# Kernel optimization log

Measured on AMD Instinct MI355X. Metric: run time of the kernel, lower is better.

Reference implementation:

```python
import jax, jax.numpy as jnp
import numpy as np

IN_F, OUT_F = 4096, 4096
IGS, OGS = 8, 1          # in_group_size, out_group_size
NCB, CBS = 1, 65536      # num_codebooks, codebook_size (2**16)
NIG, NOG = IN_F // IGS, OUT_F // OGS


def setup_inputs() -> dict:
    key = jax.random.key(0)
    k1, k2, k3, k4, k5 = jax.random.split(key, 5)
    x = jax.random.normal(k1, (4, 2048, IN_F), jnp.float32)
    codes = jax.random.randint(k2, (NOG, NIG, NCB), 0, CBS, dtype=jnp.int32)
    codebooks = jax.random.normal(k3, (NCB, CBS, OGS, IGS), jnp.float32) * 0.05
    scales = jax.random.uniform(k4, (NOG, 1, 1, 1), jnp.float32, 0.5, 1.5)
    bias = jax.random.normal(k5, (OUT_F,), jnp.float32) * 0.01
    return {"x": x, "codes": codes, "codebooks": codebooks, "scales": scales, "bias": bias}


def _dequantize_weight(codes, codebooks, scales):
    # codes: [nog, nig, ncb] int; codebooks: [ncb, cbs, ogs, igs]
    ncb, cbs, ogs, igs = codebooks.shape
    nog, nig, _ = codes.shape
    flat = codebooks.reshape(ncb, cbs, ogs * igs)
    # embedding_bag(mode='sum'): gather each codebook's vector and sum over codebooks
    gathered = flat[jnp.arange(ncb)[None, None, :], codes]  # [nog, nig, ncb, ogs*igs]
    w = gathered.sum(axis=2).reshape(nog, nig, ogs, igs)
    w = w * scales  # scales broadcasts over [nog, nig, ogs, igs]
    # [nog, nig, ogs, igs] -> [nog, ogs, nig, igs] -> [out_features, in_features]
    return w.swapaxes(1, 2).reshape(nog * ogs, nig * igs)


def reference(x, codes, codebooks, scales, bias):
    W = _dequantize_weight(codes, codebooks, scales)  # [OUT_F, IN_F]
    return x @ W.T + bias
```

## Files before the change

kernel.cpp:

```cpp
#include <hip/hip_runtime.h>
#include <hip/hip_bf16.h>

#define M_DIM 8192
#define N_DIM 4096
#define K_DIM 4096
#define NOG 4096
#define NIG 512

typedef __bf16 bf16x8 __attribute__((ext_vector_type(8)));
typedef float f32x16 __attribute__((ext_vector_type(16)));
typedef short short8 __attribute__((ext_vector_type(8)));

typedef const __attribute__((address_space(1))) void* as1_cvoid_p;
typedef __attribute__((address_space(3))) void* as3_void_p;

__device__ __forceinline__ unsigned short f2bf(float f) {
  union { float f; unsigned u; } c; c.f = f;
  unsigned u = c.u;
  return (unsigned short)((u + 0x7fffu + ((u >> 16) & 1u)) >> 16);
}

__global__ __launch_bounds__(256) void cvt_x_kernel(const float* __restrict__ x,
                                                    unsigned short* __restrict__ xb,
                                                    int n8) {
  int i = blockIdx.x * blockDim.x + threadIdx.x;
  int stride = gridDim.x * blockDim.x;
  for (; i < n8; i += stride) {
    const float4* p = (const float4*)(x) + (size_t)i * 2;
    float4 a = p[0], b = p[1];
    short8 o;
    o[0] = (short)f2bf(a.x); o[1] = (short)f2bf(a.y);
    o[2] = (short)f2bf(a.z); o[3] = (short)f2bf(a.w);
    o[4] = (short)f2bf(b.x); o[5] = (short)f2bf(b.y);
    o[6] = (short)f2bf(b.z); o[7] = (short)f2bf(b.w);
    ((short8*)xb)[i] = o;
  }
}

__global__ __launch_bounds__(256) void dequant_kernel(const int* __restrict__ codes,
                                                      const float* __restrict__ cb,
                                                      unsigned short* __restrict__ wb) {
  int idx = blockIdx.x * blockDim.x + threadIdx.x;
  int code = codes[idx];
  const float4* p = (const float4*)(cb + (size_t)code * 8);
  float4 a = p[0], b = p[1];
  short8 o;
  o[0] = (short)f2bf(a.x); o[1] = (short)f2bf(a.y);
  o[2] = (short)f2bf(a.z); o[3] = (short)f2bf(a.w);
  o[4] = (short)f2bf(b.x); o[5] = (short)f2bf(b.y);
  o[6] = (short)f2bf(b.z); o[7] = (short)f2bf(b.w);
  ((short8*)wb)[idx] = o;
}


#define BAR() __builtin_amdgcn_s_barrier()
#define SB() __builtin_amdgcn_sched_barrier(0)
#define PRIO1() __builtin_amdgcn_s_setprio(1)
#define PRIO0() __builtin_amdgcn_s_setprio(0)
#define LGKM(N_) asm volatile("s_waitcnt lgkmcnt(" #N_ ")" ::: "memory")
#define VMC(N_) asm volatile("s_waitcnt vmcnt(" #N_ ")" ::: "memory")

#define STAGE_P(G_, isB_, slot_, p_, kt_) do { \
  _Pragma("unroll") for (int i_ = 0; i_ < 2; ++i_) { \
    const unsigned short* src_ = (G_) + (size_t)sp_roff[i_] * 4096 + (unsigned)((kt_) + (p_) * 32) + spk; \
    __builtin_amdgcn_global_load_lds((as1_cvoid_p)src_, \
      (as3_void_p)(smem + (isB_) * 65536 + (slot_) * 32768 + (p_) * 16384 + spd[i_]), 16, 0, 0); \
  } } while (0)

#define LDA32(dst_, ks_, slot_) \
  _Pragma("unroll") for (int mf_ = 0; mf_ < 4; ++mf_) \
    dst_[mf_] = *(const bf16x8*)(smem + ((unsigned)((slot_) * 32768 + ((ks_) >> 1) * 16384 + mf_ * 2048 + aRd0) ^ (((ks_) & 1) << 5)));

#define LDB32(dst_, ks_, slot_) \
  _Pragma("unroll") for (int nf_ = 0; nf_ < 2; ++nf_) \
    dst_[nf_] = *(const bf16x8*)(smem + ((unsigned)(65536 + (slot_) * 32768 + ((ks_) >> 1) * 16384 + nf_ * 2048 + bRd0) ^ (((ks_) & 1) << 5)));

#define MFMA8(af_, bf_) \
  _Pragma("unroll") for (int mf_ = 0; mf_ < 4; ++mf_) \
  _Pragma("unroll") for (int nf_ = 0; nf_ < 2; ++nf_) \
    acc[mf_][nf_] = __builtin_amdgcn_mfma_f32_32x32x16_bf16(af_[mf_], bf_[nf_], acc[mf_][nf_], 0, 0, 0);

#define GROUP32(S_, MODE_, KT_) do { \
   \
  if ((MODE_) == 2) STAGE_P(Ag, 0, (S_) ^ 1, 0, (KT_) + 64); \
  LDA32(afA, 0, S_); LDB32(bfA, 0, S_); SB(); \
  LDA32(afB, 1, S_); LDB32(bfB, 1, S_); SB(); \
  LGKM(6); SB(); PRIO1(); MFMA8(afA, bfA); PRIO0(); SB(); \
   \
  if ((MODE_) == 2) STAGE_P(Bg, 1, (S_) ^ 1, 0, (KT_) + 64); \
  LGKM(0); SB(); PRIO1(); MFMA8(afB, bfB); PRIO0(); SB(); \
  if ((MODE_) == 2) { VMC(4); } else { VMC(0); } \
  BAR(); \
   \
  if ((MODE_) == 2) STAGE_P(Ag, 0, (S_) ^ 1, 1, (KT_) + 64); \
  LDA32(afA, 2, S_); LDB32(bfA, 2, S_); SB(); \
  LDA32(afB, 3, S_); LDB32(bfB, 3, S_); SB(); \
  LGKM(6); SB(); PRIO1(); MFMA8(afA, bfA); PRIO0(); SB(); \
   \
  if ((MODE_) == 2) STAGE_P(Bg, 1, (S_) ^ 1, 1, (KT_) + 64); \
  LGKM(0); SB(); PRIO1(); MFMA8(afB, bfB); PRIO0(); SB(); \
  if ((MODE_) == 2) { VMC(4); BAR(); } \
} while (0)

__global__ __launch_bounds__(512) void gemm8_kernel(
    const unsigned short* __restrict__ A,
    const unsigned short* __restrict__ B,
    const float* __restrict__ scales,
    const float* __restrict__ bias,
    float* __restrict__ C) {
  extern __shared__ char smem[];

  const int bid = blockIdx.x;
  const int swz = (bid & 7) * 64 + (bid >> 3);
  const int bm = swz >> 4;
  const int bn = swz & 15;

  const int tid = threadIdx.x;
  const int w = tid >> 6;
  const int l = tid & 63;
  const int wr = w >> 2;
  const int wcol = w & 3;

  const int llog3 = (l & 3) ^ (((l >> 5) & 1) << 1);
  const int spk = llog3 * 8;
  int sp_roff[2], spd[2];
#pragma unroll
  for (int i = 0; i < 2; ++i) {
    sp_roff[i] = w * 32 + i * 16 + (l >> 2);
    spd[i] = (w * 128 + i * 64 + l) * 16;
  }

  const unsigned short* Ag = A + (size_t)bm * 256 * 4096;
  const unsigned short* Bg = B + (size_t)bn * 256 * 4096;

  const int xr0 = ((l >> 5) * 16) + (((l >> 3) & 1) << 5);
  const int aRd0 = (wr * 128 + (l & 31)) * 64 + xr0;
  const int bRd0 = (wcol * 64 + (l & 31)) * 64 + xr0;

  f32x16 acc[4][2];
#pragma unroll
  for (int mf = 0; mf < 4; ++mf)
#pragma unroll
    for (int nf = 0; nf < 2; ++nf)
#pragma unroll
      for (int r = 0; r < 16; ++r) acc[mf][nf][r] = 0.f;

  bf16x8 afA[4], afB[4], bfA[2], bfB[2];

  STAGE_P(Ag, 0, 0, 0, 0); STAGE_P(Bg, 1, 0, 0, 0);
  STAGE_P(Ag, 0, 0, 1, 0); STAGE_P(Bg, 1, 0, 1, 0);
  VMC(4);
  BAR();

  int kt = 0;
  for (int j = 0; j < 31; ++j) {
    GROUP32(0, 2, kt);
    GROUP32(1, 2, kt + 64);
    kt += 128;
  }
  GROUP32(0, 2, 3968);
  GROUP32(1, 0, 4032);

  const int r0 = bm * 256 + wr * 128 + 4 * (l >> 5);
  const int c0 = bn * 256 + wcol * 64 + (l & 31);
#pragma unroll
  for (int nf = 0; nf < 2; ++nf) {
    const int col = c0 + nf * 32;
    const float s = scales[col];
    const float bv = bias[col];
#pragma unroll
    for (int mf = 0; mf < 4; ++mf) {
      f32x16 v = acc[mf][nf];
      const int rb = r0 + mf * 32;
#pragma unroll
      for (int r = 0; r < 16; ++r)
        C[(size_t)(rb + (r & 3) + 8 * (r >> 2)) * 4096 + col] = v[r] * s + bv;
    }
  }
}

extern "C" void kernel_launch(void* const* d_in, const int* in_sizes, int n_in,
                              void* d_out, int out_size, void* d_ws, size_t ws_size,
                              hipStream_t stream) {
  const float* x = (const float*)d_in[0];
  const int* codes = (const int*)d_in[1];
  const float* cb = (const float*)d_in[2];
  const float* scales = (const float*)d_in[3];
  const float* bias = (const float*)d_in[4];
  float* out = (float*)d_out;

  unsigned short* xb = (unsigned short*)d_ws;
  unsigned short* wb = (unsigned short*)((char*)d_ws + (size_t)M_DIM * K_DIM * 2);

  hipFuncSetAttribute((const void*)gemm8_kernel,
                      hipFuncAttributeMaxDynamicSharedMemorySize, 131072);

  cvt_x_kernel<<<4096, 256, 0, stream>>>(x, xb, (M_DIM * K_DIM) / 8);
  dequant_kernel<<<(NOG * NIG) / 256, 256, 0, stream>>>(codes, cb, wb);
  gemm8_kernel<<<dim3((M_DIM / 256) * (N_DIM / 256)), 512, 131072, stream>>>(
      xb, wb, scales, bias, out);
}
```

Measured before the change: 298.7 us.

## Restructure LDS layout into per-k-step slabs and software-pipeline fragment loads

Changes the shared-memory staging layout so each 16-wide k slice is stored as a contiguous slab, with rows indexed directly and no XOR swizzle. Global-to-LDS copies are split into four quarter stages interleaved with the four MFMA sub-steps. The first fragments of the next slot are prefetched before the last MFMA batch, so LDS reads overlap compute. This adds more barriers per group, and removing the swizzle may cause LDS bank conflicts on the read side.

```diff
diff --git a/kernel.cpp b/kernel.cpp
--- a/kernel.cpp
+++ b/kernel.cpp
@@ -60,20 +60,19 @@
 #define LGKM(N_) asm volatile("s_waitcnt lgkmcnt(" #N_ ")" ::: "memory")
 #define VMC(N_) asm volatile("s_waitcnt vmcnt(" #N_ ")" ::: "memory")
 
-#define STAGE_P(G_, isB_, slot_, p_, kt_) do { \
-  _Pragma("unroll") for (int i_ = 0; i_ < 2; ++i_) { \
-    const unsigned short* src_ = (G_) + (size_t)sp_roff[i_] * 4096 + (unsigned)((kt_) + (p_) * 32) + spk; \
-    __builtin_amdgcn_global_load_lds((as1_cvoid_p)src_, \
-      (as3_void_p)(smem + (isB_) * 65536 + (slot_) * 32768 + (p_) * 16384 + spd[i_]), 16, 0, 0); \
-  } } while (0)
+#define STAGE_I(G_, isB_, slot_, i_, kt_) do { \
+  const unsigned short* src_ = (G_) + (size_t)(srow0 + l) * 4096 + (unsigned)((kt_) + (i_) * 16 + shalf8); \
+  __builtin_amdgcn_global_load_lds((as1_cvoid_p)src_, \
+    (as3_void_p)(smem + (isB_) * 65536 + (slot_) * 32768 + ((i_) * 8 + w) * 1024), 16, 0, 0); \
+} while (0)
 
 #define LDA32(dst_, ks_, slot_) \
   _Pragma("unroll") for (int mf_ = 0; mf_ < 4; ++mf_) \
-    dst_[mf_] = *(const bf16x8*)(smem + ((unsigned)((slot_) * 32768 + ((ks_) >> 1) * 16384 + mf_ * 2048 + aRd0) ^ (((ks_) & 1) << 5)));
+    dst_[mf_] = *(const bf16x8*)(smem + (slot_) * 32768 + (ks_) * 8192 + aRd0 + mf_ * 512);
 
 #define LDB32(dst_, ks_, slot_) \
   _Pragma("unroll") for (int nf_ = 0; nf_ < 2; ++nf_) \
-    dst_[nf_] = *(const bf16x8*)(smem + ((unsigned)(65536 + (slot_) * 32768 + ((ks_) >> 1) * 16384 + nf_ * 2048 + bRd0) ^ (((ks_) & 1) << 5)));
+    dst_[nf_] = *(const bf16x8*)(smem + 65536 + (slot_) * 32768 + (ks_) * 8192 + bRd0 + nf_ * 512);
 
 #define MFMA8(af_, bf_) \
   _Pragma("unroll") for (int mf_ = 0; mf_ < 4; ++mf_) \
@@ -82,24 +81,31 @@
 
 #define GROUP32(S_, MODE_, KT_) do { \
    \
-  if ((MODE_) == 2) STAGE_P(Ag, 0, (S_) ^ 1, 0, (KT_) + 64); \
-  LDA32(afA, 0, S_); LDB32(bfA, 0, S_); SB(); \
+  if ((MODE_) == 2) { STAGE_I(Ag, 0, (S_) ^ 1, 0, (KT_) + 64); STAGE_I(Bg, 1, (S_) ^ 1, 0, (KT_) + 64); } \
   LDA32(afB, 1, S_); LDB32(bfB, 1, S_); SB(); \
   LGKM(6); SB(); PRIO1(); MFMA8(afA, bfA); PRIO0(); SB(); \
-   \
-  if ((MODE_) == 2) STAGE_P(Bg, 1, (S_) ^ 1, 0, (KT_) + 64); \
-  LGKM(0); SB(); PRIO1(); MFMA8(afB, bfB); PRIO0(); SB(); \
+  if ((MODE_) == 2) { VMC(4); } else { VMC(2); } \
+  BAR(); \
+   \
+  if ((MODE_) == 2) { STAGE_I(Ag, 0, (S_) ^ 1, 1, (KT_) + 64); STAGE_I(Bg, 1, (S_) ^ 1, 1, (KT_) + 64); } \
+  LDA32(afA, 2, S_); LDB32(bfA, 2, S_); SB(); \
+  LGKM(6); SB(); PRIO1(); MFMA8(afB, bfB); PRIO0(); SB(); \
   if ((MODE_) == 2) { VMC(4); } else { VMC(0); } \
   BAR(); \
    \
-  if ((MODE_) == 2) STAGE_P(Ag, 0, (S_) ^ 1, 1, (KT_) + 64); \
-  LDA32(afA, 2, S_); LDB32(bfA, 2, S_); SB(); \
+  if ((MODE_) == 2) { STAGE_I(Ag, 0, (S_) ^ 1, 2, (KT_) + 64); STAGE_I(Bg, 1, (S_) ^ 1, 2, (KT_) + 64); } \
   LDA32(afB, 3, S_); LDB32(bfB, 3, S_); SB(); \
   LGKM(6); SB(); PRIO1(); MFMA8(afA, bfA); PRIO0(); SB(); \
-   \
-  if ((MODE_) == 2) STAGE_P(Bg, 1, (S_) ^ 1, 1, (KT_) + 64); \
-  LGKM(0); SB(); PRIO1(); MFMA8(afB, bfB); PRIO0(); SB(); \
-  if ((MODE_) == 2) { VMC(4); BAR(); } \
+  if ((MODE_) == 2) { VMC(4); } \
+  BAR(); \
+   \
+  if ((MODE_) == 2) { STAGE_I(Ag, 0, (S_) ^ 1, 3, (KT_) + 64); STAGE_I(Bg, 1, (S_) ^ 1, 3, (KT_) + 64); } \
+  if ((MODE_) == 2) { LDA32(afA, 0, (S_) ^ 1); LDB32(bfA, 0, (S_) ^ 1); } \
+  SB(); \
+  if ((MODE_) == 2) { LGKM(6); } else { LGKM(0); } \
+  SB(); PRIO1(); MFMA8(afB, bfB); PRIO0(); SB(); \
+  if ((MODE_) == 2) { VMC(4); } \
+  BAR(); \
 } while (0)
 
 __global__ __launch_bounds__(512) void gemm8_kernel(
@@ -121,21 +127,14 @@
   const int wr = w >> 2;
   const int wcol = w & 3;
 
-  const int llog3 = (l & 3) ^ (((l >> 5) & 1) << 1);
-  const int spk = llog3 * 8;
-  int sp_roff[2], spd[2];
-#pragma unroll
-  for (int i = 0; i < 2; ++i) {
-    sp_roff[i] = w * 32 + i * 16 + (l >> 2);
-    spd[i] = (w * 128 + i * 64 + l) * 16;
-  }
+  const int srow0 = (w & 3) * 64;
+  const int shalf8 = ((w >> 2) & 1) * 8;
 
   const unsigned short* Ag = A + (size_t)bm * 256 * 4096;
   const unsigned short* Bg = B + (size_t)bn * 256 * 4096;
 
-  const int xr0 = ((l >> 5) * 16) + (((l >> 3) & 1) << 5);
-  const int aRd0 = (wr * 128 + (l & 31)) * 64 + xr0;
-  const int bRd0 = (wcol * 64 + (l & 31)) * 64 + xr0;
+  const int aRd0 = ((l >> 5) * 4096) + (wr * 128 + (l & 31)) * 16;
+  const int bRd0 = ((l >> 5) * 4096) + (wcol * 64 + (l & 31)) * 16;
 
   f32x16 acc[4][2];
 #pragma unroll
@@ -147,10 +146,13 @@
 
   bf16x8 afA[4], afB[4], bfA[2], bfB[2];
 
-  STAGE_P(Ag, 0, 0, 0, 0); STAGE_P(Bg, 1, 0, 0, 0);
-  STAGE_P(Ag, 0, 0, 1, 0); STAGE_P(Bg, 1, 0, 1, 0);
+  STAGE_I(Ag, 0, 0, 0, 0); STAGE_I(Bg, 1, 0, 0, 0);
+  STAGE_I(Ag, 0, 0, 1, 0); STAGE_I(Bg, 1, 0, 1, 0);
+  STAGE_I(Ag, 0, 0, 2, 0); STAGE_I(Bg, 1, 0, 2, 0);
+  STAGE_I(Ag, 0, 0, 3, 0); STAGE_I(Bg, 1, 0, 3, 0);
   VMC(4);
   BAR();
+  LDA32(afA, 0, 0); LDB32(bfA, 0, 0); SB();
 
   int kt = 0;
   for (int j = 0; j < 31; ++j) {
```

New measurement: 561.3 us. 87.9% more time.
